# Kernel optimization log

Hardware: AMD Instinct MI355X
Metric: run time of the kernel (lower is better)

Reference implementation:

```python
import jax, jax.numpy as jnp
import numpy as np

NSUB = 2          # fixed RK4 substeps per output interval (deterministic stand-in for adaptive dopri5)
SLOPE = 1.0 / 5.5  # leaky_relu negative slope used by g and OutputNN


def setup_inputs() -> dict:
    key = jax.random.key(0)
    ks = iter(jax.random.split(key, 40))
    B, Tp, Tf = 256, 32, 256
    D, H, HF, HG, HO = 1, 100, 275, 75, 75

    def rn(shape, s=0.05):
        return jax.random.normal(next(ks), shape, jnp.float32) * s

    # past: [B, Tp, 1+D] with strictly increasing times in column 0
    past_t = jnp.sort(jax.random.uniform(next(ks), (B, Tp), jnp.float32) * Tp, axis=1)
    past_x = jax.random.normal(next(ks), (B, Tp, D), jnp.float32)
    past = jnp.concatenate([past_t[:, :, None], past_x], axis=2)
    # future times start after the last past time, strictly increasing
    t_future = past_t[:, -1:] + jnp.sort(
        jax.random.uniform(next(ks), (B, Tf), jnp.float32) * 0.1 * Tf, axis=1)

    return dict(
        past=past,
        h0=jnp.zeros((B, H), jnp.float32),
        t_future=t_future,
        eps=jax.random.normal(next(ks), (H, B), jnp.float32),
        fW1=rn((HF, H + 1)), fb1=rn((HF,)), fW2=rn((HF, HF)), fb2=rn((HF,)),
        fW3=rn((H, HF)), fb3=rn((H,)),
        gru_Wih=rn((3 * H, D)), gru_Whh=rn((3 * H, H)),
        gru_bih=rn((3 * H,)), gru_bhh=rn((3 * H,)),
        gW1=rn((HG, H)), gb1=rn((HG,)), gW2=rn((HG, HG)), gb2=rn((HG,)),
        gW3=rn((2, HG)), gb3=rn((2,)),
        oW1=rn((HO, H)), ob1=rn((HO,)), oW2=rn((HO, HO)), ob2=rn((HO,)),
        oW3=rn((D, HO)), ob3=rn((D,)),
    )


def _leaky(x):
    return jnp.where(x >= 0, x, SLOPE * x)


def reference(past, h0, t_future, eps,
              fW1, fb1, fW2, fb2, fW3, fb3,
              gru_Wih, gru_Whh, gru_bih, gru_bhh,
              gW1, gb1, gW2, gb2, gW3, gb3,
              oW1, ob1, oW2, ob2, oW3, ob3):
    def field(t, y):  # t: [B], y: [B, H] -> dy/dt: [B, H]  (f module)
        x = jnp.concatenate([t[:, None], y], axis=1)
        x = jnp.tanh(x @ fW1.T + fb1)
        x = jnp.tanh(x @ fW2.T + fb2)
        return jnp.tanh(x @ fW3.T + fb3)

    def integrate(y0, t0, t1):  # batched fixed-step RK4 from t0 to t1 (per-batch times)
        dt = ((t1 - t0) / NSUB)[:, None]  # [B, 1]
        dts = dt[:, 0]
        def body(y, i):
            t = t0 + i * dts
            k1 = field(t, y)
            k2 = field(t + 0.5 * dts, y + 0.5 * dt * k1)
            k3 = field(t + 0.5 * dts, y + 0.5 * dt * k2)
            k4 = field(t + dts, y + dt * k3)
            return y + dt * (k1 + 2.0 * k2 + 2.0 * k3 + k4) / 6.0, None
        y, _ = jax.lax.scan(body, y0, jnp.arange(NSUB, dtype=y0.dtype))
        return y

    def gru(x, h):  # torch.nn.GRUCell math
        gi = x @ gru_Wih.T + gru_bih
        gh = h @ gru_Whh.T + gru_bhh
        ir, iz, inn = jnp.split(gi, 3, axis=1)
        hr, hz, hn = jnp.split(gh, 3, axis=1)
        r = jax.nn.sigmoid(ir + hr)
        z = jax.nn.sigmoid(iz + hz)
        n = jnp.tanh(inn + r * hn)
        return (1.0 - z) * n + z * h

    times = past[:, :, 0]   # [B, Tp]
    data = past[:, :, 1:]   # [B, Tp, D]

    # first GRUODE step: evolve h0 from t0-1 to t0, then GRU update with x0
    h = gru(data[:, 0], integrate(h0, times[:, 0] - 1.0, times[:, 0]))
    xs = (jnp.swapaxes(data[:, 1:], 0, 1), times[:, :-1].T, times[:, 1:].T)
    def pbody(hc, s):
        x, tp, tc = s
        return gru(x, integrate(hc, tp, tc)), None
    h, _ = jax.lax.scan(pbody, h, xs)

    # g head -> (loc, |scale|), reproducing the concat/view of the original
    gx = _leaky(h @ gW1.T + gb1)
    gx = _leaky(gx @ gW2.T + gb2)
    gx = gx @ gW3.T + gb3                                   # [B, 2]
    pr = jnp.concatenate([gx[:, 0], jnp.abs(gx[:, 1])]).reshape(-1, 2)
    loc, scale = pr[:, 0], pr[:, 1]                          # [B], [B]

    # Sampler: Normal(loc, scale).rsample([H]) reparameterized with eps [H, B]
    z0 = (loc[None, :] + scale[None, :] * eps).T             # [B, H]

    # integrate z0 across future time grid
    def fbody(y, s):
        tp, tc = s
        yn = integrate(y, tp, tc)
        return yn, yn
    _, traj = jax.lax.scan(fbody, z0, (t_future[:, :-1].T, t_future[:, 1:].T))
    out = jnp.swapaxes(jnp.concatenate([z0[None], traj], axis=0), 0, 1)  # [B, Tf, H]

    # OutputNN head
    o = _leaky(out @ oW1.T + ob1)
    o = _leaky(o @ oW2.T + ob2)
    return o @ oW3.T + ob3  # [B, Tf, D]
```

## Files before the change

kernel.cpp:

```cpp
#include <hip/hip_runtime.h>
#include <hip/hip_fp16.h>

typedef _Float16 f16;
typedef _Float16 f16x2 __attribute__((ext_vector_type(2)));
typedef _Float16 f16x8 __attribute__((ext_vector_type(8)));
typedef float f32x4 __attribute__((ext_vector_type(4)));
typedef unsigned short u16;
typedef unsigned int u32;

__device__ __forceinline__ float fdot2v(f16x2 a, f16x2 b, float c){
#if __has_builtin(__builtin_amdgcn_fdot2)
  return __builtin_amdgcn_fdot2(a, b, c, false);
#else
  return c + (float)a.x * (float)b.x + (float)a.y * (float)b.y;
#endif
}

__device__ __forceinline__ float tanh_f(float x){
  return 1.f - 2.f / (__expf(2.f * x) + 1.f);
}
__device__ __forceinline__ float sigm_f(float x){
  return 1.f / (1.f + __expf(-x));
}
__device__ __forceinline__ float leaky_f(float x){
  return x >= 0.f ? x : x * (1.0f / 5.5f);
}

template<int NP>
__device__ __forceinline__ void ld_pairs(const float* W, int row, int ncols, int c0,
                                         f16x2* dst, bool valid){
  const float* base = W + (long)row * ncols;
#pragma unroll
  for (int p = 0; p < NP; p++){
    int c = c0 + 2 * p;
    f16x2 v;
    v.x = (valid && c     < ncols) ? (f16)base[c]     : (f16)0.f;
    v.y = (valid && c + 1 < ncols) ? (f16)base[c + 1] : (f16)0.f;
    dst[p] = v;
  }
}

template<int NCH>
__device__ __forceinline__ float dot_chunks(const f16x2* w, const f16x8* x, int chunk0){
  float a0 = 0.f, a1 = 0.f, a2 = 0.f, a3 = 0.f;
#pragma unroll
  for (int c = 0; c < NCH; c++){
    union { f16x8 v; f16x2 h[4]; } u;
    u.v = x[chunk0 + c];
    a0 = fdot2v(w[4*c + 0], u.h[0], a0);
    a1 = fdot2v(w[4*c + 1], u.h[1], a1);
    a2 = fdot2v(w[4*c + 2], u.h[2], a2);
    a3 = fdot2v(w[4*c + 3], u.h[3], a3);
  }
  return (a0 + a1) + (a2 + a3);
}

__device__ __forceinline__ f16x8 ldfrag(const float* W, int row, int ncols, int k0, bool valid){
  f16x8 v;
#pragma unroll
  for (int j = 0; j < 8; j++){
    int c = k0 + j;
    v[j] = (valid && c < ncols) ? (f16)W[(long)row * ncols + c] : (f16)0.f;
  }
  return v;
}

__device__ __forceinline__ float sel4(f32x4 a, int c){
  float v = a.x;
  v = (c == 1) ? a.y : v;
  v = (c == 2) ? a.z : v;
  v = (c == 3) ? a.w : v;
  return v;
}

#define MFMA16(A,B,C) __builtin_amdgcn_mfma_f32_16x16x32_f16((A),(B),(C),0,0,0)

struct FRM {
  f16x8 a1[2][4];
  f16x8 a2[2][9];
  f16x8 a3[9];
  f16x2 w1b[4];
  f16x2 w2b[9];
  float w1tb, b1bv, b2bv;
  float w1tw0, w1tw1, b1w0, b1w1, b2w0, b2w1, b3w;
};

__device__ __forceinline__ void load_field_mfma(FRM& R, int tid,
    const float* fW1, const float* fb1, const float* fW2, const float* fb2,
    const float* fW3, const float* fb3)
{
  const int lane = tid & 63, wv = tid >> 6;
  const int lm = lane & 15, lg = lane >> 4;
  const int r0 = 32 * wv + lm, r1 = r0 + 16;
#pragma unroll
  for (int c = 0; c < 4; c++){
    R.a1[0][c] = ldfrag(fW1, r0, 101, 32 * c + 8 * lg, true);
    R.a1[1][c] = ldfrag(fW1, r1, 101, 32 * c + 8 * lg, true);
  }
#pragma unroll
  for (int c = 0; c < 9; c++){
    R.a2[0][c] = ldfrag(fW2, r0, 275, 32 * c + 8 * lg, true);
    R.a2[1][c] = ldfrag(fW2, r1, 275, 32 * c + 8 * lg, true);
  }
  const int r3 = 16 * wv + lm;
  const bool v3 = (wv < 7) && (r3 < 100);
#pragma unroll
  for (int c = 0; c < 9; c++)
    R.a3[c] = ldfrag(fW3, v3 ? r3 : 0, 275, 32 * c + 8 * lg, v3);

  const bool p2 = tid < 304;
  const int m = tid >> 4, s = tid & 15;
  const int j2 = 256 + m;
  ld_pairs<4>(fW1, p2 ? j2 : 0, 101, 8 * s, R.w1b, p2);
  R.w1tb = (p2 && s == 0) ? fW1[j2 * 101] : 0.f;
  R.b1bv = p2 ? fb1[j2] : 0.f;
  ld_pairs<9>(fW2, p2 ? j2 : 0, 275, 18 * s, R.w2b, p2);
  R.b2bv = p2 ? fb2[j2] : 0.f;

  const int rwc = 32 * wv + 4 * lg + (lm & 3);
  R.w1tw0 = fW1[rwc * 101];          R.w1tw1 = fW1[(rwc + 16) * 101];
  R.b1w0  = fb1[rwc];                R.b1w1  = fb1[rwc + 16];
  R.b2w0  = fb2[rwc];                R.b2w1  = fb2[rwc + 16];
  const int r3w = 16 * wv + 4 * lg + (lm & 3);
  R.b3w = ((wv < 7) && (r3w < 100)) ? fb3[r3w] : 0.f;
}

__device__ __forceinline__ f32x4 field_eval_m(const FRM& R, float t, int tid,
    f16* ust, f16* x1s, f16* x2s)
{
  const int lm = tid & 15, lg = (tid >> 4) & 3, wv = tid >> 6;
  const f16x8* ub  = (const f16x8*)ust;
  const f16x8* x1b = (const f16x8*)x1s;
  const f16x8* x2b = (const f16x8*)x2s;
  const f32x4 zz = {0.f, 0.f, 0.f, 0.f};

  f32x4 acc0 = zz, acc1 = zz;
#pragma unroll
  for (int c = 0; c < 4; c++){
    f16x8 bf = ub[4 * c + lg];
    acc0 = MFMA16(R.a1[0][c], bf, acc0);
    acc1 = MFMA16(R.a1[1][c], bf, acc1);
  }
  if (tid < 304){
    int s = tid & 15;
    float a2 = (s == 0) ? R.w1tb * t : 0.f;
    const f16x2* uv2 = (const f16x2*)ust + 4 * s;
#pragma unroll
    for (int p = 0; p < 4; p++) a2 = fdot2v(R.w1b[p], uv2[p], a2);
    a2 += __shfl_xor(a2, 1); a2 += __shfl_xor(a2, 2);
    a2 += __shfl_xor(a2, 4); a2 += __shfl_xor(a2, 8);
    if (s == 0) x1s[256 + (tid >> 4)] = (f16)tanh_f(a2 + R.b1bv);
  }
  if (lm < 4){
    int rw = 32 * wv + 4 * lg + lm;
    x1s[rw]      = (f16)tanh_f(sel4(acc0, lm) + R.w1tw0 * t + R.b1w0);
    x1s[rw + 16] = (f16)tanh_f(sel4(acc1, lm) + R.w1tw1 * t + R.b1w1);
  }
  __syncthreads();

  acc0 = zz; acc1 = zz;
#pragma unroll
  for (int c = 0; c < 9; c++){
    f16x8 bf = x1b[4 * c + lg];
    acc0 = MFMA16(R.a2[0][c], bf, acc0);
    acc1 = MFMA16(R.a2[1][c], bf, acc1);
  }
  if (tid < 304){
    int s = tid & 15;
    float a2 = 0.f;
    const f16x2* xv2 = (const f16x2*)x1s + 9 * s;
#pragma unroll
    for (int p = 0; p < 9; p++) a2 = fdot2v(R.w2b[p], xv2[p], a2);
    a2 += __shfl_xor(a2, 1); a2 += __shfl_xor(a2, 2);
    a2 += __shfl_xor(a2, 4); a2 += __shfl_xor(a2, 8);
    if (s == 0) x2s[256 + (tid >> 4)] = (f16)tanh_f(a2 + R.b2bv);
  }
  if (lm < 4){
    int rw = 32 * wv + 4 * lg + lm;
    x2s[rw]      = (f16)tanh_f(sel4(acc0, lm) + R.b2w0);
    x2s[rw + 16] = (f16)tanh_f(sel4(acc1, lm) + R.b2w1);
  }
  __syncthreads();

  f32x4 acc3 = zz;
  if (wv < 7){
#pragma unroll
    for (int c = 0; c < 9; c++)
      acc3 = MFMA16(R.a3[c], x2b[4 * c + lg], acc3);
  }
  return acc3;
}

__global__ __launch_bounds__(512, 2) void k_encode(
    const float* __restrict__ past, const float* __restrict__ h0,
    const float* __restrict__ fW1, const float* __restrict__ fb1,
    const float* __restrict__ fW2, const float* __restrict__ fb2,
    const float* __restrict__ fW3, const float* __restrict__ fb3,
    const float* __restrict__ Wih, const float* __restrict__ Whh,
    const float* __restrict__ bih, const float* __restrict__ bhh,
    const float* __restrict__ gW1, const float* __restrict__ gb1,
    const float* __restrict__ gW2, const float* __restrict__ gb2,
    const float* __restrict__ gW3, const float* __restrict__ gb3,
    float* __restrict__ gx_ws)
{
  __shared__ f16x8 ustV[16];
  __shared__ f16x8 ystV[16];
  __shared__ f16x8 x1V[36];
  __shared__ f16x8 x2V[36];
  __shared__ float yf[100];
  __shared__ float ghs[300];
  __shared__ f16x2 gW1s[75 * 52];
  __shared__ f16x2 gW2s[75 * 40];
  __shared__ f16x2 gW3s[80];
  __shared__ f16x2 g1s2[40];
  __shared__ f16x2 g2s2[40];

  const int tid = threadIdx.x;
  const int b = blockIdx.x;
  f16* ust = (f16*)ustV;
  f16* yst = (f16*)ystV;
  f16* x1s = (f16*)x1V;
  f16* x2s = (f16*)x2V;
  f16* g1s = (f16*)g1s2;
  f16* g2s = (f16*)g2s2;

  FRM R;
  load_field_mfma(R, tid, fW1, fb1, fW2, fb2, fW3, fb3);

  f16x2 whh[28]; float bhhv;
  f16x2 whhb[7]; float bhhbv;
  {
    int j1 = tid >> 1, h = tid & 1;
    ld_pairs<28>(Whh, j1, 100, 56 * h, whh, true);
    bhhv = bhh[j1];
    bool p2 = tid < 352;
    int j2 = 256 + (tid >> 3), s7 = tid & 7;
    ld_pairs<7>(Whh, p2 ? j2 : 0, 100, 14 * s7, whhb, p2);
    bhhbv = p2 ? bhh[j2] : 0.f;
  }
  float wihr=0,wihz=0,wihn=0,bihr=0,bihz=0,bihn=0;
  if (tid < 100){
    wihr = Wih[tid];       bihr = bih[tid];
    wihz = Wih[tid + 100]; bihz = bih[tid + 100];
    wihn = Wih[tid + 200]; bihn = bih[tid + 200];
  }
  const int jq = tid >> 2, qq = tid & 3;
  const bool lv = (qq == 0 && jq < 75);
  float gb1v = lv ? gb1[jq] : 0.f;
  float gb2v = lv ? gb2[jq] : 0.f;

  for (int i = tid; i < 75 * 52; i += 512){
    int r = i / 52, c = 2 * (i % 52);
    f16x2 v;
    v.x = (c     < 100) ? (f16)gW1[r * 100 + c]     : (f16)0.f;
    v.y = (c + 1 < 100) ? (f16)gW1[r * 100 + c + 1] : (f16)0.f;
    gW1s[i] = v;
  }
  for (int i = tid; i < 75 * 40; i += 512){
    int r = i / 40, c = 2 * (i % 40);
    f16x2 v;
    v.x = (c     < 75) ? (f16)gW2[r * 75 + c]     : (f16)0.f;
    v.y = (c + 1 < 75) ? (f16)gW2[r * 75 + c + 1] : (f16)0.f;
    gW2s[i] = v;
  }
  for (int i = tid; i < 80; i += 512){
    int r = i / 40, c = 2 * (i % 40);
    f16x2 v;
    v.x = (c     < 75) ? (f16)gW3[r * 75 + c]     : (f16)0.f;
    v.y = (c + 1 < 75) ? (f16)gW3[r * 75 + c + 1] : (f16)0.f;
    gW3s[i] = v;
  }
  for (int i = tid; i < 128; i += 512){ ust[i] = (f16)0.f; yst[i] = (f16)0.f; }
  for (int i = tid; i < 288; i += 512){ x1s[i] = (f16)0.f; x2s[i] = (f16)0.f; }
  for (int i = tid; i < 80;  i += 512){ g1s[i] = (f16)0.f; g2s[i] = (f16)0.f; }
  if (tid < 100){
    float v = h0[b * 100 + tid];
    yf[tid] = v; yst[tid] = (f16)v; ust[1 + tid] = (f16)v;
  }
  __syncthreads();

  const int lm = tid & 15, lg = (tid >> 4) & 3, wv = tid >> 6;
  const int row3 = 16 * wv + 4 * lg + (lm & 3);
  const bool wr3 = (lm < 4) && (wv < 7) && (row3 < 100);
  float k1v = 0.f, k2v = 0.f, k3v = 0.f, yfr = 0.f;

  auto rk_interval = [&](float tp, float tc){
    float dts = (tc - tp) * 0.5f;
#pragma unroll 1
    for (int sub = 0; sub < 2; sub++){
      float t0 = tp + sub * dts;
      __syncthreads();
      if (wr3) yfr = yf[row3];
      f32x4 a = field_eval_m(R, t0, tid, ust, x1s, x2s);
      if (wr3){ float kv = tanh_f(sel4(a, lm) + R.b3w); k1v = kv;
                ust[1 + row3] = (f16)(yfr + 0.5f * dts * kv); }
      __syncthreads();
      a = field_eval_m(R, t0 + 0.5f * dts, tid, ust, x1s, x2s);
      if (wr3){ float kv = tanh_f(sel4(a, lm) + R.b3w); k2v = kv;
                ust[1 + row3] = (f16)(yfr + 0.5f * dts * kv); }
      __syncthreads();
      a = field_eval_m(R, t0 + 0.5f * dts, tid, ust, x1s, x2s);
      if (wr3){ float kv = tanh_f(sel4(a, lm) + R.b3w); k3v = kv;
                ust[1 + row3] = (f16)(yfr + dts * kv); }
      __syncthreads();
      a = field_eval_m(R, t0 + dts, tid, ust, x1s, x2s);
      if (wr3){
        float kv = tanh_f(sel4(a, lm) + R.b3w);
        float yn = yfr + dts * (k1v + 2.f * (k2v + k3v) + kv) * (1.f / 6.f);
        yf[row3] = yn; ust[1 + row3] = (f16)yn; yst[row3] = (f16)yn;
      }
    }
  };

  const float* prow = past + b * 64;
#pragma unroll 1
  for (int st = 0; st < 32; st++){
    float tc = prow[2 * st];
    float tp = (st == 0) ? (tc - 1.f) : prow[2 * st - 2];
    rk_interval(tp, tc);
    __syncthreads();
    {
      int j1 = tid >> 1, h = tid & 1;
      float a = dot_chunks<7>(whh, ystV, 7 * h);
      a += __shfl_xor(a, 1);
      if (!h) ghs[j1] = a + bhhv;
      if (tid < 352){
        int s7 = tid & 7;
        float a2 = 0.f;
        const f16x2* yv2 = (const f16x2*)ystV + 7 * s7;
#pragma unroll
        for (int p = 0; p < 7; p++) a2 = fdot2v(whhb[p], yv2[p], a2);
        a2 += __shfl_xor(a2, 1); a2 += __shfl_xor(a2, 2); a2 += __shfl_xor(a2, 4);
        if (s7 == 0) ghs[256 + (tid >> 3)] = a2 + bhhbv;
      }
    }
    __syncthreads();
    if (tid < 100){
      float x = prow[2 * st + 1];
      float r = sigm_f(x * wihr + bihr + ghs[tid]);
      float z = sigm_f(x * wihz + bihz + ghs[tid + 100]);
      float n = tanh_f(x * wihn + bihn + r * ghs[tid + 200]);
      float hn = (1.f - z) * n + z * yf[tid];
      yf[tid] = hn; yst[tid] = (f16)hn; ust[1 + tid] = (f16)hn;
    }
  }

  __syncthreads();
  {
    float a = 0.f;
    const f16x2* yv = (const f16x2*)ystV + 13 * qq;
    if (jq < 75){
#pragma unroll
      for (int p = 0; p < 13; p++) a = fdot2v(gW1s[jq * 52 + 13 * qq + p], yv[p], a);
    }
    a += __shfl_xor(a, 1); a += __shfl_xor(a, 2);
    if (lv) g1s[jq] = (f16)leaky_f(a + gb1v);
  }
  __syncthreads();
  {
    float a = 0.f;
    const f16x2* xv = (const f16x2*)g1s + 10 * qq;
    if (jq < 75){
#pragma unroll
      for (int p = 0; p < 10; p++) a = fdot2v(gW2s[jq * 40 + 10 * qq + p], xv[p], a);
    }
    a += __shfl_xor(a, 1); a += __shfl_xor(a, 2);
    if (lv) g2s[jq] = (f16)leaky_f(a + gb2v);
  }
  __syncthreads();
  if (tid < 2){
    const f16x2* g2v = (const f16x2*)g2s;
    float a = gb3[tid];
    for (int p = 0; p < 40; p++) a = fdot2v(gW3s[tid * 40 + p], g2v[p], a);
    gx_ws[b * 2 + tid] = a;
  }
}

__global__ __launch_bounds__(512, 2) void k_forecast(
    const float* __restrict__ t_future, const float* __restrict__ eps,
    const float* __restrict__ fW1, const float* __restrict__ fb1,
    const float* __restrict__ fW2, const float* __restrict__ fb2,
    const float* __restrict__ fW3, const float* __restrict__ fb3,
    const float* __restrict__ oW1, const float* __restrict__ ob1,
    const float* __restrict__ oW2, const float* __restrict__ ob2,
    const float* __restrict__ oW3, const float* __restrict__ ob3,
    const float* __restrict__ gx_ws, float* __restrict__ out)
{
  __shared__ f16x8 ustV[16];
  __shared__ f16x8 ystV[16];
  __shared__ f16x8 x1V[36];
  __shared__ f16x8 x2V[36];
  __shared__ f16x8 o1V[12];
  __shared__ f16x8 o2V[12];

  const int tid = threadIdx.x;
  const int b = blockIdx.x;
  f16* ust = (f16*)ustV;
  f16* yst = (f16*)ystV;
  f16* x1s = (f16*)x1V;
  f16* x2s = (f16*)x2V;
  f16* o1s = (f16*)o1V;
  f16* o2s = (f16*)o2V;

  FRM R;
  load_field_mfma(R, tid, fW1, fb1, fW2, fb2, fW3, fb3);

  const int jq = tid >> 2, qq = tid & 3;
  const bool dv = jq < 75;
  const bool lv = (qq == 0 && dv);
  f16x2 dW1[16]; f16x2 dW2[12]; f16x2 dW3;
  ld_pairs<16>(oW1, dv ? jq : 0, 100, 32 * qq, dW1, dv);
  ld_pairs<12>(oW2, dv ? jq : 0, 75, 24 * qq, dW2, dv);
  ld_pairs<1>(oW3, 0, 75, 2 * tid, &dW3, tid < 40);
  float ob1v = lv ? ob1[jq] : 0.f;
  float ob2v = lv ? ob2[jq] : 0.f;
  float ob3v = ob3[0];

  for (int i = tid; i < 128; i += 512){ ust[i] = (f16)0.f; yst[i] = (f16)0.f; }
  for (int i = tid; i < 288; i += 512){ x1s[i] = (f16)0.f; x2s[i] = (f16)0.f; }
  for (int i = tid; i < 96;  i += 512){ o1s[i] = (f16)0.f; o2s[i] = (f16)0.f; }

  const int lm = tid & 15, lg = (tid >> 4) & 3, wv = tid >> 6;
  const int row3 = 16 * wv + 4 * lg + (lm & 3);
  const bool wr3 = (lm < 4) && (wv < 7) && (row3 < 100);
  float k1v = 0.f, k2v = 0.f, k3v = 0.f, yfr = 0.f;

  if (wr3){
    float loc, scl;
    if (b < 128){ loc = gx_ws[4 * b];              scl = gx_ws[4 * b + 2]; }
    else        { loc = fabsf(gx_ws[4 * b - 511]); scl = fabsf(gx_ws[4 * b - 509]); }
    float e = eps[row3 * 256 + b];
    yfr = loc + scl * e;
    yst[row3] = (f16)yfr; ust[1 + row3] = (f16)yfr;
  }
  __syncthreads();

  auto decode = [&](int tf){
    {
      float a = 0.f;
      if (dv) a = dot_chunks<4>(dW1, ystV, 4 * qq);
      a += __shfl_xor(a, 1); a += __shfl_xor(a, 2);
      if (lv) o1s[jq] = (f16)leaky_f(a + ob1v);
    }
    __syncthreads();
    {
      float a = 0.f;
      if (dv) a = dot_chunks<3>(dW2, o1V, 3 * qq);
      a += __shfl_xor(a, 1); a += __shfl_xor(a, 2);
      if (lv) o2s[jq] = (f16)leaky_f(a + ob2v);
    }
    __syncthreads();
    if (tid < 64){
      float a = 0.f;
      if (tid < 40) a = fdot2v(dW3, ((const f16x2*)o2V)[tid], 0.f);
      a += __shfl_xor(a, 1);  a += __shfl_xor(a, 2);  a += __shfl_xor(a, 4);
      a += __shfl_xor(a, 8);  a += __shfl_xor(a, 16); a += __shfl_xor(a, 32);
      if (tid == 0) out[b * 256 + tf] = a + ob3v;
    }
  };

  decode(0);

  const float* trow = t_future + b * 256;
#pragma unroll 1
  for (int iv = 0; iv < 255; iv++){
    float tp = trow[iv];
    float tc = trow[iv + 1];
    float dts = (tc - tp) * 0.5f;
#pragma unroll 1
    for (int sub = 0; sub < 2; sub++){
      float t0 = tp + sub * dts;
      __syncthreads();
      f32x4 a = field_eval_m(R, t0, tid, ust, x1s, x2s);
      if (wr3){ float kv = tanh_f(sel4(a, lm) + R.b3w); k1v = kv;
                ust[1 + row3] = (f16)(yfr + 0.5f * dts * kv); }
      __syncthreads();
      a = field_eval_m(R, t0 + 0.5f * dts, tid, ust, x1s, x2s);
      if (wr3){ float kv = tanh_f(sel4(a, lm) + R.b3w); k2v = kv;
                ust[1 + row3] = (f16)(yfr + 0.5f * dts * kv); }
      __syncthreads();
      a = field_eval_m(R, t0 + 0.5f * dts, tid, ust, x1s, x2s);
      if (wr3){ float kv = tanh_f(sel4(a, lm) + R.b3w); k3v = kv;
                ust[1 + row3] = (f16)(yfr + dts * kv); }
      __syncthreads();
      a = field_eval_m(R, t0 + dts, tid, ust, x1s, x2s);
      if (wr3){
        float kv = tanh_f(sel4(a, lm) + R.b3w);
        float yn = yfr + dts * (k1v + 2.f * (k2v + k3v) + kv) * (1.f / 6.f);
        yfr = yn; ust[1 + row3] = (f16)yn; yst[row3] = (f16)yn;
      }
    }
    __syncthreads();
    decode(iv + 1);
  }
}

extern "C" void kernel_launch(void* const* d_in, const int* in_sizes, int n_in,
                              void* d_out, int out_size, void* d_ws, size_t ws_size,
                              hipStream_t stream) {
  (void)in_sizes; (void)n_in; (void)out_size; (void)ws_size;
  const float* past     = (const float*)d_in[0];
  const float* h0       = (const float*)d_in[1];
  const float* t_future = (const float*)d_in[2];
  const float* eps      = (const float*)d_in[3];
  const float* fW1 = (const float*)d_in[4];  const float* fb1 = (const float*)d_in[5];
  const float* fW2 = (const float*)d_in[6];  const float* fb2 = (const float*)d_in[7];
  const float* fW3 = (const float*)d_in[8];  const float* fb3 = (const float*)d_in[9];
  const float* Wih = (const float*)d_in[10]; const float* Whh = (const float*)d_in[11];
  const float* bih = (const float*)d_in[12]; const float* bhh = (const float*)d_in[13];
  const float* gW1 = (const float*)d_in[14]; const float* gb1 = (const float*)d_in[15];
  const float* gW2 = (const float*)d_in[16]; const float* gb2 = (const float*)d_in[17];
  const float* gW3 = (const float*)d_in[18]; const float* gb3 = (const float*)d_in[19];
  const float* oW1 = (const float*)d_in[20]; const float* ob1 = (const float*)d_in[21];
  const float* oW2 = (const float*)d_in[22]; const float* ob2 = (const float*)d_in[23];
  const float* oW3 = (const float*)d_in[24]; const float* ob3 = (const float*)d_in[25];
  float* gxws = (float*)d_ws;
  float* out = (float*)d_out;

  hipLaunchKernelGGL(k_encode, dim3(256), dim3(512), 0, stream,
      past, h0, fW1, fb1, fW2, fb2, fW3, fb3,
      Wih, Whh, bih, bhh, gW1, gb1, gW2, gb2, gW3, gb3, gxws);
  hipLaunchKernelGGL(k_forecast, dim3(256), dim3(512), 0, stream,
      t_future, eps, fW1, fb1, fW2, fb2, fW3, fb3,
      oW1, ob1, oW2, ob2, oW3, ob3, gxws, out);
}
```

Before: 4.254 ms.

## Fuse output decoder into first RK stage and split MFMA accumulation chains

Folds the per-timestep OutputNN decode into the first field evaluation of each interval, so its three layers run alongside the field MLP stages and reuse their barriers rather than adding three extra syncs per interval. The last timestep's decode moves after the loop. It also splits each MFMA reduction into two independent accumulator chains to shorten dependency latency, and spreads the activation epilogue across 8 lanes instead of 4 to halve serial tanh work. Division is replaced by a hardware reciprocal in tanh and sigmoid. This adds register pressure from holding decoder weights in a struct, slightly lowers reciprocal precision, and changes the lane mapping, which could introduce bugs.

```diff
diff --git a/kernel.cpp b/kernel.cpp
--- a/kernel.cpp
+++ b/kernel.cpp
@@ -16,11 +16,19 @@
 #endif
 }
 
+__device__ __forceinline__ float rcp_f(float x){
+#if __has_builtin(__builtin_amdgcn_rcpf)
+  return __builtin_amdgcn_rcpf(x);
+#else
+  return 1.f / x;
+#endif
+}
+
 __device__ __forceinline__ float tanh_f(float x){
-  return 1.f - 2.f / (__expf(2.f * x) + 1.f);
+  return 1.f - 2.f * rcp_f(__expf(2.f * x) + 1.f);
 }
 __device__ __forceinline__ float sigm_f(float x){
-  return 1.f / (1.f + __expf(-x));
+  return rcp_f(1.f + __expf(-x));
 }
 __device__ __forceinline__ float leaky_f(float x){
   return x >= 0.f ? x : x * (1.0f / 5.5f);
@@ -72,6 +80,14 @@
   v = (c == 3) ? a.w : v;
   return v;
 }
+__device__ __forceinline__ float selacc(f32x4 a0, f32x4 a1, int lm){
+  f32x4 t;
+  t.x = (lm & 4) ? a1.x : a0.x;
+  t.y = (lm & 4) ? a1.y : a0.y;
+  t.z = (lm & 4) ? a1.z : a0.z;
+  t.w = (lm & 4) ? a1.w : a0.w;
+  return sel4(t, lm & 3);
+}
 
 #define MFMA16(A,B,C) __builtin_amdgcn_mfma_f32_16x16x32_f16((A),(B),(C),0,0,0)
 
@@ -82,7 +98,13 @@
   f16x2 w1b[4];
   f16x2 w2b[9];
   float w1tb, b1bv, b2bv;
-  float w1tw0, w1tw1, b1w0, b1w1, b2w0, b2w1, b3w;
+  float w1tw, b1w, b2w;
+  float b3w;
+};
+
+struct DEC {
+  f16x2 dW1[16]; f16x2 dW2[12]; f16x2 dW3;
+  float ob1v, ob2v, ob3v;
 };
 
 __device__ __forceinline__ void load_field_mfma(FRM& R, int tid,
@@ -117,16 +139,19 @@
   ld_pairs<9>(fW2, p2 ? j2 : 0, 275, 18 * s, R.w2b, p2);
   R.b2bv = p2 ? fb2[j2] : 0.f;
 
-  const int rwc = 32 * wv + 4 * lg + (lm & 3);
-  R.w1tw0 = fW1[rwc * 101];          R.w1tw1 = fW1[(rwc + 16) * 101];
-  R.b1w0  = fb1[rwc];                R.b1w1  = fb1[rwc + 16];
-  R.b2w0  = fb2[rwc];                R.b2w1  = fb2[rwc + 16];
+  const int lmw = lm & 7;
+  const int rwc = 32 * wv + 16 * (lmw >> 2) + 4 * lg + (lmw & 3);
+  R.w1tw = fW1[rwc * 101];
+  R.b1w  = fb1[rwc];
+  R.b2w  = fb2[rwc];
   const int r3w = 16 * wv + 4 * lg + (lm & 3);
   R.b3w = ((wv < 7) && (r3w < 100)) ? fb3[r3w] : 0.f;
 }
 
-__device__ __forceinline__ f32x4 field_eval_m(const FRM& R, float t, int tid,
-    f16* ust, f16* x1s, f16* x2s)
+template<bool D>
+__device__ __forceinline__ f32x4 field_eval_m(const FRM& R, const DEC& dc,
+    float t, int tid, f16* ust, f16* x1s, f16* x2s,
+    const f16x8* yv, f16* o1s, f16* o2s, float* outp, int tf)
 {
   const int lm = tid & 15, lg = (tid >> 4) & 3, wv = tid >> 6;
   const f16x8* ub  = (const f16x8*)ust;
@@ -134,59 +159,107 @@
   const f16x8* x2b = (const f16x8*)x2s;
   const f32x4 zz = {0.f, 0.f, 0.f, 0.f};
 
-  f32x4 acc0 = zz, acc1 = zz;
-#pragma unroll
-  for (int c = 0; c < 4; c++){
-    f16x8 bf = ub[4 * c + lg];
-    acc0 = MFMA16(R.a1[0][c], bf, acc0);
-    acc1 = MFMA16(R.a1[1][c], bf, acc1);
-  }
-  if (tid < 304){
-    int s = tid & 15;
-    float a2 = (s == 0) ? R.w1tb * t : 0.f;
-    const f16x2* uv2 = (const f16x2*)ust + 4 * s;
-#pragma unroll
-    for (int p = 0; p < 4; p++) a2 = fdot2v(R.w1b[p], uv2[p], a2);
-    a2 += __shfl_xor(a2, 1); a2 += __shfl_xor(a2, 2);
-    a2 += __shfl_xor(a2, 4); a2 += __shfl_xor(a2, 8);
-    if (s == 0) x1s[256 + (tid >> 4)] = (f16)tanh_f(a2 + R.b1bv);
-  }
-  if (lm < 4){
-    int rw = 32 * wv + 4 * lg + lm;
-    x1s[rw]      = (f16)tanh_f(sel4(acc0, lm) + R.w1tw0 * t + R.b1w0);
-    x1s[rw + 16] = (f16)tanh_f(sel4(acc1, lm) + R.w1tw1 * t + R.b1w1);
-  }
-  __syncthreads();
-
-  acc0 = zz; acc1 = zz;
-#pragma unroll
-  for (int c = 0; c < 9; c++){
-    f16x8 bf = x1b[4 * c + lg];
-    acc0 = MFMA16(R.a2[0][c], bf, acc0);
-    acc1 = MFMA16(R.a2[1][c], bf, acc1);
-  }
-  if (tid < 304){
-    int s = tid & 15;
-    float a2 = 0.f;
-    const f16x2* xv2 = (const f16x2*)x1s + 9 * s;
-#pragma unroll
-    for (int p = 0; p < 9; p++) a2 = fdot2v(R.w2b[p], xv2[p], a2);
-    a2 += __shfl_xor(a2, 1); a2 += __shfl_xor(a2, 2);
-    a2 += __shfl_xor(a2, 4); a2 += __shfl_xor(a2, 8);
-    if (s == 0) x2s[256 + (tid >> 4)] = (f16)tanh_f(a2 + R.b2bv);
-  }
-  if (lm < 4){
-    int rw = 32 * wv + 4 * lg + lm;
-    x2s[rw]      = (f16)tanh_f(sel4(acc0, lm) + R.b2w0);
-    x2s[rw + 16] = (f16)tanh_f(sel4(acc1, lm) + R.b2w1);
+  {
+    f32x4 p0 = zz, p1 = zz, q0 = zz, q1 = zz;
+#pragma unroll
+    for (int c = 0; c < 2; c++){
+      f16x8 bp = ub[4 * c + lg];
+      f16x8 bq = ub[4 * (c + 2) + lg];
+      p0 = MFMA16(R.a1[0][c],     bp, p0);
+      p1 = MFMA16(R.a1[1][c],     bp, p1);
+      q0 = MFMA16(R.a1[0][c + 2], bq, q0);
+      q1 = MFMA16(R.a1[1][c + 2], bq, q1);
+    }
+    if (tid < 304){
+      int s = tid & 15;
+      float a2 = (s == 0) ? R.w1tb * t : 0.f;
+      const f16x2* uv2 = (const f16x2*)ust + 4 * s;
+#pragma unroll
+      for (int p = 0; p < 4; p++) a2 = fdot2v(R.w1b[p], uv2[p], a2);
+      a2 += __shfl_xor(a2, 1); a2 += __shfl_xor(a2, 2);
+      a2 += __shfl_xor(a2, 4); a2 += __shfl_xor(a2, 8);
+      if (s == 0) x1s[256 + (tid >> 4)] = (f16)tanh_f(a2 + R.b1bv);
+    }
+    if (D){
+      int jq = tid >> 2, qq = tid & 3;
+      if (jq < 75){
+        float a = dot_chunks<4>(dc.dW1, yv, 4 * qq);
+        a += __shfl_xor(a, 1); a += __shfl_xor(a, 2);
+        if (qq == 0) o1s[jq] = (f16)leaky_f(a + dc.ob1v);
+      }
+    }
+    f32x4 acc0 = p0 + q0, acc1 = p1 + q1;
+    if (lm < 8){
+      int rw = 32 * wv + 16 * (lm >> 2) + 4 * lg + (lm & 3);
+      float v = selacc(acc0, acc1, lm);
+      x1s[rw] = (f16)tanh_f(v + R.w1tw * t + R.b1w);
+    }
+  }
+  __syncthreads();
+
+  {
+    f32x4 p0 = zz, p1 = zz, q0 = zz, q1 = zz;
+#pragma unroll
+    for (int c = 0; c < 4; c++){
+      f16x8 bp = x1b[4 * c + lg];
+      f16x8 bq = x1b[4 * (c + 5) + lg];
+      p0 = MFMA16(R.a2[0][c],     bp, p0);
+      p1 = MFMA16(R.a2[1][c],     bp, p1);
+      q0 = MFMA16(R.a2[0][c + 5], bq, q0);
+      q1 = MFMA16(R.a2[1][c + 5], bq, q1);
+    }
+    {
+      f16x8 bp = x1b[16 + lg];
+      p0 = MFMA16(R.a2[0][4], bp, p0);
+      p1 = MFMA16(R.a2[1][4], bp, p1);
+    }
+    if (tid < 304){
+      int s = tid & 15;
+      float a2 = 0.f;
+      const f16x2* xv2 = (const f16x2*)x1s + 9 * s;
+#pragma unroll
+      for (int p = 0; p < 9; p++) a2 = fdot2v(R.w2b[p], xv2[p], a2);
+      a2 += __shfl_xor(a2, 1); a2 += __shfl_xor(a2, 2);
+      a2 += __shfl_xor(a2, 4); a2 += __shfl_xor(a2, 8);
+      if (s == 0) x2s[256 + (tid >> 4)] = (f16)tanh_f(a2 + R.b2bv);
+    }
+    if (D){
+      int jq = tid >> 2, qq = tid & 3;
+      if (jq < 75){
+        float a = dot_chunks<3>(dc.dW2, (const f16x8*)o1s, 3 * qq);
+        a += __shfl_xor(a, 1); a += __shfl_xor(a, 2);
+        if (qq == 0) o2s[jq] = (f16)leaky_f(a + dc.ob2v);
+      }
+    }
+    f32x4 acc0 = p0 + q0, acc1 = p1 + q1;
+    if (lm < 8){
+      int rw = 32 * wv + 16 * (lm >> 2) + 4 * lg + (lm & 3);
+      float v = selacc(acc0, acc1, lm);
+      x2s[rw] = (f16)tanh_f(v + R.b2w);
+    }
   }
   __syncthreads();
 
   f32x4 acc3 = zz;
   if (wv < 7){
-#pragma unroll
-    for (int c = 0; c < 9; c++)
-      acc3 = MFMA16(R.a3[c], x2b[4 * c + lg], acc3);
+    f32x4 r0 = zz, r1 = zz;
+#pragma unroll
+    for (int c = 0; c < 4; c++){
+      r0 = MFMA16(R.a3[c],     x2b[4 * c + lg], r0);
+      r1 = MFMA16(R.a3[c + 5], x2b[4 * (c + 5) + lg], r1);
+    }
+    r0 = MFMA16(R.a3[4], x2b[16 + lg], r0);
+    acc3 = r0 + r1;
+  }
+  if (D){
+    if (tid >= 448){
+      int t2 = tid - 448;
+      float a = 0.f;
+      if (t2 < 40) a = fdot2v(dc.dW3, ((const f16x2*)o2s)[t2], 0.f);
+      a += __shfl_xor(a, 1);  a += __shfl_xor(a, 2);  a += __shfl_xor(a, 4);
+      a += __shfl_xor(a, 8);  a += __shfl_xor(a, 16); a += __shfl_xor(a, 32);
+      if (t2 == 0) outp[tf] = a + dc.ob3v;
+    }
   }
   return acc3;
 }
@@ -226,6 +299,7 @@
 
   FRM R;
   load_field_mfma(R, tid, fW1, fb1, fW2, fb2, fW3, fb3);
+  DEC dcz{};
 
   f16x2 whh[28]; float bhhv;
   f16x2 whhb[7]; float bhhbv;
@@ -279,31 +353,36 @@
   }
   __syncthreads();
 
-  const int lm = tid & 15, lg = (tid >> 4) & 3, wv = tid >> 6;
-  const int row3 = 16 * wv + 4 * lg + (lm & 3);
+  const int lm = tid & 15, lg2 = (tid >> 4) & 3, wv = tid >> 6;
+  const int row3 = 16 * wv + 4 * lg2 + (lm & 3);
   const bool wr3 = (lm < 4) && (wv < 7) && (row3 < 100);
-  float k1v = 0.f, k2v = 0.f, k3v = 0.f, yfr = 0.f;
+  float k1v = 0.f, k2v = 0.f, k3v = 0.f;
 
   auto rk_interval = [&](float tp, float tc){
     float dts = (tc - tp) * 0.5f;
 #pragma unroll 1
     for (int sub = 0; sub < 2; sub++){
       float t0 = tp + sub * dts;
+      float yfr = 0.f;
       __syncthreads();
       if (wr3) yfr = yf[row3];
-      f32x4 a = field_eval_m(R, t0, tid, ust, x1s, x2s);
+      f32x4 a = field_eval_m<false>(R, dcz, t0, tid, ust, x1s, x2s,
+                                    nullptr, nullptr, nullptr, nullptr, 0);
       if (wr3){ float kv = tanh_f(sel4(a, lm) + R.b3w); k1v = kv;
                 ust[1 + row3] = (f16)(yfr + 0.5f * dts * kv); }
       __syncthreads();
-      a = field_eval_m(R, t0 + 0.5f * dts, tid, ust, x1s, x2s);
+      a = field_eval_m<false>(R, dcz, t0 + 0.5f * dts, tid, ust, x1s, x2s,
+                              nullptr, nullptr, nullptr, nullptr, 0);
       if (wr3){ float kv = tanh_f(sel4(a, lm) + R.b3w); k2v = kv;
                 ust[1 + row3] = (f16)(yfr + 0.5f * dts * kv); }
       __syncthreads();
-      a = field_eval_m(R, t0 + 0.5f * dts, tid, ust, x1s, x2s);
+      a = field_eval_m<false>(R, dcz, t0 + 0.5f * dts, tid, ust, x1s, x2s,
+                              nullptr, nullptr, nullptr, nullptr, 0);
       if (wr3){ float kv = tanh_f(sel4(a, lm) + R.b3w); k3v = kv;
                 ust[1 + row3] = (f16)(yfr + dts * kv); }
       __syncthreads();
-      a = field_eval_m(R, t0 + dts, tid, ust, x1s, x2s);
+      a = field_eval_m<false>(R, dcz, t0 + dts, tid, ust, x1s, x2s,
+                              nullptr, nullptr, nullptr, nullptr, 0);
       if (wr3){
         float kv = tanh_f(sel4(a, lm) + R.b3w);
         float yn = yfr + dts * (k1v + 2.f * (k2v + k3v) + kv) * (1.f / 6.f);
@@ -401,6 +480,7 @@
   f16* x2s = (f16*)x2V;
   f16* o1s = (f16*)o1V;
   f16* o2s = (f16*)o2V;
+  float* outb = out + b * 256;
 
   FRM R;
   load_field_mfma(R, tid, fW1, fb1, fW2, fb2, fW3, fb3);
@@ -408,20 +488,24 @@
   const int jq = tid >> 2, qq = tid & 3;
   const bool dv = jq < 75;
   const bool lv = (qq == 0 && dv);
-  f16x2 dW1[16]; f16x2 dW2[12]; f16x2 dW3;
-  ld_pairs<16>(oW1, dv ? jq : 0, 100, 32 * qq, dW1, dv);
-  ld_pairs<12>(oW2, dv ? jq : 0, 75, 24 * qq, dW2, dv);
-  ld_pairs<1>(oW3, 0, 75, 2 * tid, &dW3, tid < 40);
-  float ob1v = lv ? ob1[jq] : 0.f;
-  float ob2v = lv ? ob2[jq] : 0.f;
-  float ob3v = ob3[0];
+  DEC dc;
+  ld_pairs<16>(oW1, dv ? jq : 0, 100, 32 * qq, dc.dW1, dv);
+  ld_pairs<12>(oW2, dv ? jq : 0, 75, 24 * qq, dc.dW2, dv);
+  {
+    int t2 = tid - 448;
+    bool v = (t2 >= 0 && t2 < 40);
+    ld_pairs<1>(oW3, 0, 75, v ? 2 * t2 : 0, &dc.dW3, v);
+  }
+  dc.ob1v = lv ? ob1[jq] : 0.f;
+  dc.ob2v = lv ? ob2[jq] : 0.f;
+  dc.ob3v = ob3[0];
 
   for (int i = tid; i < 128; i += 512){ ust[i] = (f16)0.f; yst[i] = (f16)0.f; }
   for (int i = tid; i < 288; i += 512){ x1s[i] = (f16)0.f; x2s[i] = (f16)0.f; }
   for (int i = tid; i < 96;  i += 512){ o1s[i] = (f16)0.f; o2s[i] = (f16)0.f; }
 
-  const int lm = tid & 15, lg = (tid >> 4) & 3, wv = tid >> 6;
-  const int row3 = 16 * wv + 4 * lg + (lm & 3);
+  const int lm = tid & 15, lg2 = (tid >> 4) & 3, wv = tid >> 6;
+  const int row3 = 16 * wv + 4 * lg2 + (lm & 3);
   const bool wr3 = (lm < 4) && (wv < 7) && (row3 < 100);
   float k1v = 0.f, k2v = 0.f, k3v = 0.f, yfr = 0.f;
 
@@ -434,32 +518,6 @@
     yst[row3] = (f16)yfr; ust[1 + row3] = (f16)yfr;
   }
   __syncthreads();
-
-  auto decode = [&](int tf){
-    {
-      float a = 0.f;
-      if (dv) a = dot_chunks<4>(dW1, ystV, 4 * qq);
-      a += __shfl_xor(a, 1); a += __shfl_xor(a, 2);
-      if (lv) o1s[jq] = (f16)leaky_f(a + ob1v);
-    }
-    __syncthreads();
-    {
-      float a = 0.f;
-      if (dv) a = dot_chunks<3>(dW2, o1V, 3 * qq);
-      a += __shfl_xor(a, 1); a += __shfl_xor(a, 2);
-      if (lv) o2s[jq] = (f16)leaky_f(a + ob2v);
-    }
-    __syncthreads();
-    if (tid < 64){
-      float a = 0.f;
-      if (tid < 40) a = fdot2v(dW3, ((const f16x2*)o2V)[tid], 0.f);
-      a += __shfl_xor(a, 1);  a += __shfl_xor(a, 2);  a += __shfl_xor(a, 4);
-      a += __shfl_xor(a, 8);  a += __shfl_xor(a, 16); a += __shfl_xor(a, 32);
-      if (tid == 0) out[b * 256 + tf] = a + ob3v;
-    }
-  };
-
-  decode(0);
 
   const float* trow = t_future + b * 256;
 #pragma unroll 1
@@ -471,27 +529,56 @@
     for (int sub = 0; sub < 2; sub++){
       float t0 = tp + sub * dts;
       __syncthreads();
-      f32x4 a = field_eval_m(R, t0, tid, ust, x1s, x2s);
+      f32x4 a;
+      if (sub == 0)
+        a = field_eval_m<true >(R, dc, t0, tid, ust, x1s, x2s,
+                                (const f16x8*)yst, o1s, o2s, outb, iv);
+      else
+        a = field_eval_m<false>(R, dc, t0, tid, ust, x1s, x2s,
+                                nullptr, nullptr, nullptr, nullptr, 0);
       if (wr3){ float kv = tanh_f(sel4(a, lm) + R.b3w); k1v = kv;
                 ust[1 + row3] = (f16)(yfr + 0.5f * dts * kv); }
       __syncthreads();
-      a = field_eval_m(R, t0 + 0.5f * dts, tid, ust, x1s, x2s);
+      a = field_eval_m<false>(R, dc, t0 + 0.5f * dts, tid, ust, x1s, x2s,
+                              nullptr, nullptr, nullptr, nullptr, 0);
       if (wr3){ float kv = tanh_f(sel4(a, lm) + R.b3w); k2v = kv;
                 ust[1 + row3] = (f16)(yfr + 0.5f * dts * kv); }
       __syncthreads();
-      a = field_eval_m(R, t0 + 0.5f * dts, tid, ust, x1s, x2s);
+      a = field_eval_m<false>(R, dc, t0 + 0.5f * dts, tid, ust, x1s, x2s,
+                              nullptr, nullptr, nullptr, nullptr, 0);
       if (wr3){ float kv = tanh_f(sel4(a, lm) + R.b3w); k3v = kv;
                 ust[1 + row3] = (f16)(yfr + dts * kv); }
       __syncthreads();
-      a = field_eval_m(R, t0 + dts, tid, ust, x1s, x2s);
+      a = field_eval_m<false>(R, dc, t0 + dts, tid, ust, x1s, x2s,
+                              nullptr, nullptr, nullptr, nullptr, 0);
       if (wr3){
         float kv = tanh_f(sel4(a, lm) + R.b3w);
         float yn = yfr + dts * (k1v + 2.f * (k2v + k3v) + kv) * (1.f / 6.f);
         yfr = yn; ust[1 + row3] = (f16)yn; yst[row3] = (f16)yn;
       }
     }
-    __syncthreads();
-    decode(iv + 1);
+  }
+
+  __syncthreads();
+  if (dv){
+    float a = dot_chunks<4>(dc.dW1, (const f16x8*)yst, 4 * qq);
+    a += __shfl_xor(a, 1); a += __shfl_xor(a, 2);
+    if (qq == 0) o1s[jq] = (f16)leaky_f(a + dc.ob1v);
+  }
+  __syncthreads();
+  if (dv){
+    float a = dot_chunks<3>(dc.dW2, (const f16x8*)o1s, 3 * qq);
+    a += __shfl_xor(a, 1); a += __shfl_xor(a, 2);
+    if (qq == 0) o2s[jq] = (f16)leaky_f(a + dc.ob2v);
+  }
+  __syncthreads();
+  if (tid >= 448){
+    int t2 = tid - 448;
+    float a = 0.f;
+    if (t2 < 40) a = fdot2v(dc.dW3, ((const f16x2*)o2s)[t2], 0.f);
+    a += __shfl_xor(a, 1);  a += __shfl_xor(a, 2);  a += __shfl_xor(a, 4);
+    a += __shfl_xor(a, 8);  a += __shfl_xor(a, 16); a += __shfl_xor(a, 32);
+    if (t2 == 0) outb[255] = a + dc.ob3v;
   }
 }
 
```

Result: faster. 3.894 ms (-8.5%).
